# Performance work log

Hardware: AMD Instinct MI355X
Metric: run time of the kernel (lower is better)

## Reference

```python
import jax, jax.numpy as jnp
import numpy as np

M = 16384      # total flat points per role (8 scenes x 2048 pts)
D = 256        # d_model
H = 4          # heads
K = 16         # knn neighbors
DFF = 1024     # 4*D
LN_EPS = 1e-5


def _ln(x, g, b):
    m = jnp.mean(x, axis=-1, keepdims=True)
    v = jnp.mean((x - m) ** 2, axis=-1, keepdims=True)
    return (x - m) / jnp.sqrt(v + LN_EPS) * g + b


def _knn_block(x, coord, ctx, ctx_coord, idx,
               Wq, Wk, Wv, Wo, g1, b1, pe_w, pe_b,
               W1, bf1, W2, bf2, g2, b2):
    # x: [M,D] query feats; ctx: [N,D] context feats; idx: [M,K] neighbor ids (-1 = invalid)
    m, d = x.shape
    k = idx.shape[1]
    dh = d // H
    valid = idx >= 0
    idx_c = jnp.where(valid, idx, 0)

    xn = _ln(x, g1, b1)
    q = (xn @ Wq).reshape(m, H, dh)                      # [M,H,dh]
    k_all = ctx @ Wk                                     # [N,D]
    v_all = ctx @ Wv                                     # [N,D]

    rel = coord[:, None, :] - ctx_coord[idx_c]           # [M,K,3]
    pe = rel @ pe_w + pe_b                               # [M,K,D] relative position encoding
    kg = (k_all[idx_c] + pe).reshape(m, k, H, dh)        # gathered keys  [M,K,H,dh]
    vg = (v_all[idx_c] + pe).reshape(m, k, H, dh)        # gathered values

    scale = jnp.asarray(1.0 / np.sqrt(dh), x.dtype)
    scores = jnp.einsum('mhd,mkhd->mhk', q, kg) * scale
    scores = jnp.where(valid[:, None, :], scores, jnp.asarray(-1e9, x.dtype))
    attn = jax.nn.softmax(scores, axis=-1)
    out = jnp.einsum('mhk,mkhd->mhd', attn, vg).reshape(m, d) @ Wo
    x = x + out
    h = jax.nn.gelu(_ln(x, g2, b2) @ W1 + bf1)
    return x + (h @ W2 + bf2)


def setup_inputs() -> dict:
    key = jax.random.key(0)
    ks = jax.random.split(key, 24)
    s = 0.02
    nblk = 2  # [0]=self(a), [1]=cross(a,b)
    inp = {
        'feat_a': jax.random.normal(ks[0], (M, D), jnp.float32),
        'coord_a': jax.random.normal(ks[1], (M, 3), jnp.float32),
        'feat_b': jax.random.normal(ks[2], (M, D), jnp.float32),
        'coord_b': jax.random.normal(ks[3], (M, 3), jnp.float32),
        'Wq': jax.random.normal(ks[4], (nblk, D, D), jnp.float32) * s,
        'Wk': jax.random.normal(ks[5], (nblk, D, D), jnp.float32) * s,
        'Wv': jax.random.normal(ks[6], (nblk, D, D), jnp.float32) * s,
        'Wo': jax.random.normal(ks[7], (nblk, D, D), jnp.float32) * s,
        'ln1_g': jnp.ones((nblk, D), jnp.float32),
        'ln1_b': jnp.zeros((nblk, D), jnp.float32),
        'pe_w': jax.random.normal(ks[8], (nblk, 3, D), jnp.float32) * s,
        'pe_b': jnp.zeros((nblk, D), jnp.float32),
        'ffn_w1': jax.random.normal(ks[9], (nblk, D, DFF), jnp.float32) * s,
        'ffn_b1': jnp.zeros((nblk, DFF), jnp.float32),
        'ffn_w2': jax.random.normal(ks[10], (nblk, DFF, D), jnp.float32) * s,
        'ffn_b2': jnp.zeros((nblk, D), jnp.float32),
        'ln2_g': jnp.ones((nblk, D), jnp.float32),
        'ln2_b': jnp.zeros((nblk, D), jnp.float32),
        'knn_a2a': jax.random.randint(ks[11], (M, K), 0, M, jnp.int64 if jax.config.jax_enable_x64 else jnp.int32),
        'knn_a2b': jax.random.randint(ks[12], (M, K), 0, M, jnp.int64 if jax.config.jax_enable_x64 else jnp.int32),
    }
    return inp


def reference(feat_a, coord_a, feat_b, coord_b,
              Wq, Wk, Wv, Wo, ln1_g, ln1_b, pe_w, pe_b,
              ffn_w1, ffn_b1, ffn_w2, ffn_b2, ln2_g, ln2_b,
              knn_a2a, knn_a2b):
    def params(i):
        return (Wq[i], Wk[i], Wv[i], Wo[i], ln1_g[i], ln1_b[i], pe_w[i], pe_b[i],
                ffn_w1[i], ffn_b1[i], ffn_w2[i], ffn_b2[i], ln2_g[i], ln2_b[i])
    # layer 'self(a)': feat[a] = block(feat[a], coord[a], knn_indexes['a2a'])
    fa = _knn_block(feat_a, coord_a, feat_a, coord_a, knn_a2a, *params(0))
    # layer 'cross(a,b)': feat[a] = block(query=feat[a], context=feat[b], knn_indexes['a2b'])
    fa = _knn_block(fa, coord_a, feat_b, coord_b, knn_a2b, *params(1))
    return fa
```

## Files before the change

### kernel.cpp

```cpp
#include <hip/hip_runtime.h>
#include <hip/hip_bf16.h>
#include <stdint.h>

#define MM 16384
#define DD 256
#define HH 4
#define KK 16
#define DFF_ 1024

typedef __attribute__((ext_vector_type(8))) short bf16x8;
typedef __attribute__((ext_vector_type(16))) float f32x16;
typedef __attribute__((ext_vector_type(2))) float f32x2;

__device__ __forceinline__ unsigned short f2bf(float f) {
    unsigned u = __builtin_bit_cast(unsigned, f);
    unsigned r = u + 0x7fffu + ((u >> 16) & 1u);
    return (unsigned short)(r >> 16);
}
__device__ __forceinline__ float bf2f(unsigned short h) {
    unsigned u = ((unsigned)h) << 16;
    return __builtin_bit_cast(float, u);
}


__global__ __launch_bounds__(256) void prep_weights(
        const float* __restrict__ Wq, const float* __restrict__ Wk,
        const float* __restrict__ Wv, const float* __restrict__ Wo,
        const float* __restrict__ W1, const float* __restrict__ W2,
        unsigned short* __restrict__ wf) {
    int t = blockIdx.x * blockDim.x + threadIdx.x;
    const float* src; unsigned short* dst;
    int kd, lg, rem, blk, e, sect;
    if (t < 131072) { sect = 0; rem = t; blk = rem >> 16; e = rem & 65535;
        src = Wq; dst = wf + blk * 65536; kd = 256; lg = 8; }
    else if (t < 262144) { sect = 1; rem = t - 131072; blk = rem >> 16; e = rem & 65535;
        src = Wk; dst = wf + 131072 + blk * 131072; kd = 256; lg = 8; }
    else if (t < 393216) { sect = 2; rem = t - 262144; blk = rem >> 16; e = rem & 65535;
        src = Wv; dst = wf + 131072 + blk * 131072; kd = 256; lg = 8; }
    else if (t < 524288) { sect = 0; rem = t - 393216; blk = rem >> 16; e = rem & 65535;
        src = Wo; dst = wf + 393216 + blk * 65536; kd = 256; lg = 8; }
    else if (t < 1048576) { sect = 0; rem = t - 524288; blk = rem >> 18; e = rem & 262143;
        src = W1; dst = wf + 524288 + blk * 262144; kd = 256; lg = 10; }
    else if (t < 1572864) { sect = 0; rem = t - 1048576; blk = rem >> 18; e = rem & 262143;
        src = W2; dst = wf + 1048576 + blk * 262144; kd = 1024; lg = 8; }
    else return;
    int k = e >> lg;
    int n = e & ((1 << lg) - 1);
    if (sect == 1) n = (n >> 2) * 8 + (n & 3);
    else if (sect == 2) n = (n >> 2) * 8 + 4 + (n & 3);
    float v = src[(size_t)blk * kd * (1 << lg) + e];
    int off = ((n >> 5) * (kd >> 4) + (k >> 4)) * 512 + (((k >> 3) & 1) * 32 + (n & 31)) * 8 + (k & 7);
    dst[off] = f2bf(v);
}

__global__ __launch_bounds__(256) void ln3_to_frag(
        const float* __restrict__ xa, const float* __restrict__ g,
        const float* __restrict__ b, const float* __restrict__ xb,
        unsigned short* __restrict__ outln, unsigned short* __restrict__ outca,
        unsigned short* __restrict__ outcb) {
    int y = blockIdx.y;
    const float* x = (y == 2) ? xb : xa;
    unsigned short* out = (y == 0) ? outln : (y == 1 ? outca : outcb);
    int apply_ln = (y == 0);
    int wave = threadIdx.x >> 6, lane = threadIdx.x & 63;
    int m = blockIdx.x * 4 + wave;
    const float4 xv = reinterpret_cast<const float4*>(x + (size_t)m * DD)[lane];
    float vals[4] = {xv.x, xv.y, xv.z, xv.w};
    int k0 = lane * 4;
    if (apply_ln) {
        float s = vals[0] + vals[1] + vals[2] + vals[3];
        float sq = vals[0]*vals[0] + vals[1]*vals[1] + vals[2]*vals[2] + vals[3]*vals[3];
        for (int o = 32; o; o >>= 1) { s += __shfl_xor(s, o, 64); sq += __shfl_xor(sq, o, 64); }
        float mean = s * (1.0f / DD);
        float var = sq * (1.0f / DD) - mean * mean;
        float rs = rsqrtf(var + 1e-5f);
        #pragma unroll
        for (int c = 0; c < 4; ++c)
            vals[c] = (vals[c] - mean) * rs * g[k0 + c] + b[k0 + c];
    }
    int chunk = ((m >> 5) * (DD >> 4) + (k0 >> 4)) * 64 + ((k0 >> 3) & 1) * 32 + (m & 31);
    ushort4 o4 = make_ushort4(f2bf(vals[0]), f2bf(vals[1]), f2bf(vals[2]), f2bf(vals[3]));
    *reinterpret_cast<ushort4*>(out + (size_t)chunk * 8 + (k0 & 7)) = o4;
}

template <int KG>
__device__ __forceinline__ void compute_tile(
        const bf16x8* __restrict__ a0, const bf16x8* __restrict__ a1,
        const bf16x8* __restrict__ b0, const bf16x8* __restrict__ b1,
        f32x16 acc[2][2]) {
    #pragma unroll 4
    for (int g = 0; g < KG; ++g) {
        bf16x8 av0 = a0[g * 64];
        bf16x8 av1 = a1[g * 64];
        bf16x8 bv0 = b0[g * 64];
        bf16x8 bv1 = b1[g * 64];
        acc[0][0] = __builtin_amdgcn_mfma_f32_32x32x16_bf16(av0, bv0, acc[0][0], 0, 0, 0);
        acc[0][1] = __builtin_amdgcn_mfma_f32_32x32x16_bf16(av0, bv1, acc[0][1], 0, 0, 0);
        acc[1][0] = __builtin_amdgcn_mfma_f32_32x32x16_bf16(av1, bv0, acc[1][0], 0, 0, 0);
        acc[1][1] = __builtin_amdgcn_mfma_f32_32x32x16_bf16(av1, bv1, acc[1][1], 0, 0, 0);
    }
}

template <int KD, int NOUT>
__global__ __launch_bounds__(256) void gemm_gelu(
        const bf16x8* __restrict__ A, const bf16x8* __restrict__ B,
        unsigned short* __restrict__ outp, const float* __restrict__ bias,
        int out_kd) {
    constexpr int KG = KD / 16;
    __shared__ float lds[4 * 1056];
    int wave = threadIdx.x >> 6, lane = threadIdx.x & 63;
    int wm = wave & 1, wn = wave >> 1;
    int mw = blockIdx.x * 64 + wm * 32;
    int nw = blockIdx.y * 128 + wn * 64;
    const bf16x8* a0 = A + ((size_t)(mw >> 5) * KG) * 64 + lane;
    const bf16x8* b0 = B + ((size_t)(nw >> 5) * KG) * 64 + lane;
    const bf16x8* b1 = b0 + (size_t)KG * 64;
    f32x16 acc[2] = {};
    #pragma unroll 4
    for (int g = 0; g < KG; ++g) {
        bf16x8 av = a0[g * 64];
        bf16x8 bv0 = b0[g * 64];
        bf16x8 bv1 = b1[g * 64];
        acc[0] = __builtin_amdgcn_mfma_f32_32x32x16_bf16(av, bv0, acc[0], 0, 0, 0);
        acc[1] = __builtin_amdgcn_mfma_f32_32x32x16_bf16(av, bv1, acc[1], 0, 0, 0);
    }
    int col = lane & 31, rq = (lane >> 5) * 4;
    float* wlds = &lds[wave * 1056];
    for (int j = 0; j < 2; ++j) {
        #pragma unroll
        for (int r = 0; r < 16; ++r) {
            int row = (r & 3) + 8 * (r >> 2) + rq;
            int n = nw + j * 32 + col;
            float v = acc[j][r] + bias[n];
            float arg = v * (1.5957691216f + 0.0713548163f * v * v);
            v = v * __frcp_rn(1.0f + __expf(-arg));
            wlds[row * 33 + col] = v;
        }
        #pragma unroll
        for (int it = 0; it < 2; ++it) {
            int task = lane + it * 64;
            int row = task >> 2, cc = task & 3;
            int m = mw + row;
            int k = nw + j * 32 + cc * 8;
            float* p = &wlds[row * 33 + cc * 8];
            unsigned short us[8];
            #pragma unroll
            for (int e = 0; e < 8; ++e) us[e] = f2bf(p[e]);
            int chunk = ((m >> 5) * (out_kd >> 4) + (k >> 4)) * 64 + ((k >> 3) & 1) * 32 + (m & 31);
            reinterpret_cast<uint4*>(outp)[chunk] = *reinterpret_cast<uint4*>(us);
        }
    }
}

template <int KD, int NOUT, bool RESID, bool BIAS>
__global__ __launch_bounds__(256) void gemm_frag64(
        const bf16x8* __restrict__ A, const bf16x8* __restrict__ B,
        float* __restrict__ outp, const float* __restrict__ resid,
        const float* __restrict__ bias) {
    constexpr int KG = KD / 16;
    int wave = threadIdx.x >> 6, lane = threadIdx.x & 63;
    int wm = wave & 1, wn = wave >> 1;
    int mw = blockIdx.x * 64 + wm * 32;
    int nw = blockIdx.y * 128 + wn * 64;
    const bf16x8* a0 = A + ((size_t)(mw >> 5) * KG) * 64 + lane;
    const bf16x8* b0 = B + ((size_t)(nw >> 5) * KG) * 64 + lane;
    const bf16x8* b1 = b0 + (size_t)KG * 64;
    f32x16 acc[2] = {};
    #pragma unroll 4
    for (int g = 0; g < KG; ++g) {
        bf16x8 av = a0[g * 64];
        bf16x8 bv0 = b0[g * 64];
        bf16x8 bv1 = b1[g * 64];
        acc[0] = __builtin_amdgcn_mfma_f32_32x32x16_bf16(av, bv0, acc[0], 0, 0, 0);
        acc[1] = __builtin_amdgcn_mfma_f32_32x32x16_bf16(av, bv1, acc[1], 0, 0, 0);
    }
    int col = lane & 31, rq = (lane >> 5) * 4;
    #pragma unroll
    for (int j = 0; j < 2; ++j) {
        #pragma unroll
        for (int r = 0; r < 16; ++r) {
            int row = (r & 3) + 8 * (r >> 2) + rq;
            int m = mw + row;
            int n = nw + j * 32 + col;
            float v = acc[j][r];
            if (BIAS) v += bias[n];
            if (RESID) v += resid[(size_t)m * NOUT + n];
            outp[(size_t)m * NOUT + n] = v;
        }
    }
}

__global__ __launch_bounds__(256) void gemm_qkv(
        const bf16x8* __restrict__ Aq, const bf16x8* __restrict__ Akv,
        const bf16x8* __restrict__ Bq, const bf16x8* __restrict__ Bkv,
        unsigned short* __restrict__ qout, unsigned char* __restrict__ kvout) {
    constexpr int KG = 16;
    int wave = threadIdx.x >> 6, lane = threadIdx.x & 63;
    int wm = wave & 1, wn = wave >> 1;
    int y = blockIdx.y;
    bool isQ = y < 2;
    const bf16x8* A = isQ ? Aq : Akv;
    const bf16x8* B = isQ ? Bq : Bkv;
    int n0 = (isQ ? y : y - 2) * 128 + wn * 64;
    int m0 = blockIdx.x * 128 + wm * 64;
    const bf16x8* a0 = A + ((size_t)(m0 >> 5) * KG) * 64 + lane;
    const bf16x8* a1 = a0 + (size_t)KG * 64;
    const bf16x8* b0 = B + ((size_t)(n0 >> 5) * KG) * 64 + lane;
    const bf16x8* b1 = b0 + (size_t)KG * 64;
    f32x16 acc[2][2] = {};
    compute_tile<KG>(a0, a1, b0, b1, acc);
    int col = lane & 31, rq = (lane >> 5) * 4;
    #pragma unroll
    for (int i = 0; i < 2; ++i)
    #pragma unroll
    for (int j = 0; j < 2; ++j)
    #pragma unroll
    for (int r = 0; r < 16; ++r) {
        int row = (r & 3) + 8 * (r >> 2) + rq;
        int m = m0 + i * 32 + row;
        int n = n0 + j * 32 + col;
        float v = acc[i][j][r];
        if (isQ) qout[(size_t)m * 256 + n] = f2bf(v);
        else kvout[(size_t)m * 512 + n] =
            (unsigned char)(__builtin_amdgcn_cvt_pk_fp8_f32(v, v, 0, false) & 0xff);
    }
}

template <int O, int N>
__device__ __forceinline__ void redstage(float* a, int lane) {
    int sel = lane & O;
    #pragma unroll
    for (int u = 0; u < N / 2; ++u) {
        float lo = a[2 * u], hi = a[2 * u + 1];
        float keep = sel ? hi : lo;
        float send = sel ? lo : hi;
        a[u] = keep + __shfl_xor(send, O, 64);
    }
}

template <int KD, bool BIAS>
__global__ __launch_bounds__(512) void gemm_ln(
        const bf16x8* __restrict__ A, const bf16x8* __restrict__ B,
        float* __restrict__ out_f32, const float* __restrict__ resid,
        const float* __restrict__ bias,
        const float* __restrict__ lng, const float* __restrict__ lnb,
        unsigned short* __restrict__ out_frag) {
    constexpr int KG = KD / 16;
    __shared__ float pstat[4][64][2];
    __shared__ float stats[64][2];
    __shared__ float tlds[8][32 * 33];
    int wave = threadIdx.x >> 6, lane = threadIdx.x & 63;
    int wm = wave >> 2, wn = wave & 3;
    int m0 = blockIdx.x * 64;
    int mw = m0 + wm * 32;
    int n0 = wn * 64;
    const bf16x8* a0 = A + ((size_t)(mw >> 5) * KG) * 64 + lane;
    const bf16x8* b0 = B + ((size_t)(n0 >> 5) * KG) * 64 + lane;
    const bf16x8* b1 = b0 + (size_t)KG * 64;
    f32x16 acc[2] = {};
    #pragma unroll 4
    for (int g = 0; g < KG; ++g) {
        bf16x8 av = a0[g * 64];
        bf16x8 bv0 = b0[g * 64];
        bf16x8 bv1 = b1[g * 64];
        acc[0] = __builtin_amdgcn_mfma_f32_32x32x16_bf16(av, bv0, acc[0], 0, 0, 0);
        acc[1] = __builtin_amdgcn_mfma_f32_32x32x16_bf16(av, bv1, acc[1], 0, 0, 0);
    }
    int col = lane & 31, rq = (lane >> 5) * 4;

    #pragma unroll
    for (int j = 0; j < 2; ++j) {
        #pragma unroll
        for (int r = 0; r < 16; ++r) {
            int row = (r & 3) + 8 * (r >> 2) + rq;
            int m = mw + row;
            int n = n0 + j * 32 + col;
            float v = acc[j][r];
            if (BIAS) v += bias[n];
            v += resid[(size_t)m * DD + n];
            out_f32[(size_t)m * DD + n] = v;
            acc[j][r] = v;
        }
    }

    {
        float ps[16];
        #pragma unroll
        for (int r = 0; r < 16; ++r)
            ps[r] = acc[0][r] + acc[1][r];
        redstage<1, 16>(ps, lane);
        redstage<2, 8>(ps, lane);
        redstage<4, 4>(ps, lane);
        redstage<8, 2>(ps, lane);
        float sum64 = ps[0] + __shfl_xor(ps[0], 16, 64);
        float qs[16];
        #pragma unroll
        for (int r = 0; r < 16; ++r) {
            float a = acc[0][r], b = acc[1][r];
            qs[r] = a * a + b * b;
        }
        redstage<1, 16>(qs, lane);
        redstage<2, 8>(qs, lane);
        redstage<4, 4>(qs, lane);
        redstage<8, 2>(qs, lane);
        float sq64 = qs[0] + __shfl_xor(qs[0], 16, 64);
        int slot = lane & 15;
        int ROW = wm * 32 + (slot & 3) + 8 * (slot >> 2) + rq;
        if ((lane & 16) == 0)
            *reinterpret_cast<float2*>(&pstat[wn][ROW][0]) = make_float2(sum64, sq64);
    }
    __syncthreads();
    if (threadIdx.x < 64) {
        int R = threadIdx.x;
        float s = 0.0f, sq = 0.0f;
        #pragma unroll
        for (int w = 0; w < 4; ++w) {
            float2 p = *reinterpret_cast<float2*>(&pstat[w][R][0]);
            s += p.x; sq += p.y;
        }
        float mean = s * (1.0f / DD);
        float var = sq * (1.0f / DD) - mean * mean;
        float rstd = rsqrtf(var + 1e-5f);
        *reinterpret_cast<float2*>(&stats[R][0]) = make_float2(mean, rstd);
    }
    __syncthreads();

    float* wlds = &tlds[wave][0];
    float mean_r[16], rstd_r[16];
    #pragma unroll
    for (int r = 0; r < 16; ++r) {
        int row = (r & 3) + 8 * (r >> 2) + rq;
        float2 st = *reinterpret_cast<float2*>(&stats[wm * 32 + row][0]);
        mean_r[r] = st.x; rstd_r[r] = st.y;
    }
    for (int j = 0; j < 2; ++j) {
        float gj = lng[n0 + j * 32 + col];
        float bj = lnb[n0 + j * 32 + col];
        #pragma unroll
        for (int r = 0; r < 16; ++r) {
            int row = (r & 3) + 8 * (r >> 2) + rq;
            float v = (acc[j][r] - mean_r[r]) * rstd_r[r] * gj + bj;
            wlds[row * 33 + col] = v;
        }
        #pragma unroll
        for (int it = 0; it < 2; ++it) {
            int task = lane + it * 64;
            int row = task >> 2, cc = task & 3;
            int m = mw + row;
            int k = n0 + j * 32 + cc * 8;
            float* p = &wlds[row * 33 + cc * 8];
            unsigned short us[8];
            #pragma unroll
            for (int e = 0; e < 8; ++e) us[e] = f2bf(p[e]);
            int chunk = ((m >> 5) * (DD >> 4) + (k >> 4)) * 64 + ((k >> 3) & 1) * 32 + (m & 31);
            *reinterpret_cast<uint4*>(out_frag + (size_t)chunk * 8) = *reinterpret_cast<uint4*>(us);
        }
    }
}

__global__ __launch_bounds__(256) void attn_kernel(
        const unsigned short* __restrict__ q, const unsigned char* __restrict__ kv,
        const float* __restrict__ coord, const float* __restrict__ ctx_coord,
        const int* __restrict__ knn,
        const float* __restrict__ pe_w, const float* __restrict__ pe_b,
        unsigned short* __restrict__ out_frag) {
    int wave = threadIdx.x >> 6, lane = threadIdx.x & 63;
    int m = blockIdx.x * 4 + wave;
    int s = lane & 15;
    int d0 = (lane >> 4) * 64 + s * 4;

    ushort4 qv4 = *reinterpret_cast<const ushort4*>(q + (size_t)m * DD + d0);
    float qx = bf2f(qv4.x), qy = bf2f(qv4.y), qz = bf2f(qv4.z), qw = bf2f(qv4.w);
    float4 pw0 = *reinterpret_cast<const float4*>(pe_w + d0);
    float4 pw1 = *reinterpret_cast<const float4*>(pe_w + DD + d0);
    float4 pw2 = *reinterpret_cast<const float4*>(pe_w + 2 * DD + d0);
    float4 pbv = *reinterpret_cast<const float4*>(pe_b + d0);

    float cx = coord[m * 3], cy = coord[m * 3 + 1], cz = coord[m * 3 + 2];
    int myidx = knn[(size_t)m * KK + s];
    int icm = myidx < 0 ? 0 : myidx;
    float rx = cx - ctx_coord[icm * 3];
    float ry = cy - ctx_coord[icm * 3 + 1];
    float rz = cz - ctx_coord[icm * 3 + 2];

    float t0 = qx * pw0.x + qy * pw0.y + qz * pw0.z + qw * pw0.w;
    float t1 = qx * pw1.x + qy * pw1.y + qz * pw1.z + qw * pw1.w;
    float t2 = qx * pw2.x + qy * pw2.y + qz * pw2.z + qw * pw2.w;
    float t3 = qx * pbv.x + qy * pbv.y + qz * pbv.z + qw * pbv.w;
    #pragma unroll
    for (int o = 1; o < 16; o <<= 1) {
        t0 += __shfl_xor(t0, o, 64);
        t1 += __shfl_xor(t1, o, 64);
        t2 += __shfl_xor(t2, o, 64);
        t3 += __shfl_xor(t3, o, 64);
    }

    float P[KK];
    unsigned vpk[KK];
    #pragma unroll
    for (int j = 0; j < KK; ++j) {
        int ij = __shfl(myidx, j, 64);
        int ic = ij < 0 ? 0 : ij;
        uint2 kvv = *reinterpret_cast<const uint2*>(kv + (size_t)ic * 512 + (d0 >> 2) * 8);
        vpk[j] = kvv.y;
        f32x2 k01 = __builtin_amdgcn_cvt_pk_f32_fp8(kvv.x, false);
        f32x2 k23 = __builtin_amdgcn_cvt_pk_f32_fp8(kvv.x, true);
        P[j] = qx * k01.x + qy * k01.y + qz * k23.x + qw * k23.y;
    }
    redstage<1, 16>(P, lane);
    redstage<2, 8>(P, lane);
    redstage<4, 4>(P, lane);
    redstage<8, 2>(P, lane);
    float corr = rx * t0 + ry * t1 + rz * t2 + t3;
    float sc_own = (myidx >= 0) ? (P[0] + corr) * 0.125f : -1e9f;

    float mx = sc_own;
    mx = fmaxf(mx, __shfl_xor(mx, 1, 64));
    mx = fmaxf(mx, __shfl_xor(mx, 2, 64));
    mx = fmaxf(mx, __shfl_xor(mx, 4, 64));
    mx = fmaxf(mx, __shfl_xor(mx, 8, 64));
    float e = __expf(sc_own - mx);
    float sum = e;
    sum += __shfl_xor(sum, 1, 64);
    sum += __shfl_xor(sum, 2, 64);
    sum += __shfl_xor(sum, 4, 64);
    sum += __shfl_xor(sum, 8, 64);
    float w_own = e * __frcp_rn(sum);

    float wrx = w_own * rx, wry = w_own * ry, wrz = w_own * rz;
    #pragma unroll
    for (int o = 1; o < 16; o <<= 1) {
        wrx += __shfl_xor(wrx, o, 64);
        wry += __shfl_xor(wry, o, 64);
        wrz += __shfl_xor(wrz, o, 64);
    }

    int gbase = lane & 48;
    float ax = 0.f, ay = 0.f, az = 0.f, aw = 0.f;
    #pragma unroll
    for (int j = 0; j < KK; ++j) {
        float wj = __shfl(w_own, gbase + j, 64);
        f32x2 v01 = __builtin_amdgcn_cvt_pk_f32_fp8(vpk[j], false);
        f32x2 v23 = __builtin_amdgcn_cvt_pk_f32_fp8(vpk[j], true);
        ax += wj * v01.x;
        ay += wj * v01.y;
        az += wj * v23.x;
        aw += wj * v23.y;
    }
    ax += wrx * pw0.x + wry * pw1.x + wrz * pw2.x + pbv.x;
    ay += wrx * pw0.y + wry * pw1.y + wrz * pw2.y + pbv.y;
    az += wrx * pw0.z + wry * pw1.z + wrz * pw2.z + pbv.z;
    aw += wrx * pw0.w + wry * pw1.w + wrz * pw2.w + pbv.w;

    ushort4 o4 = make_ushort4(f2bf(ax), f2bf(ay), f2bf(az), f2bf(aw));
    int chunk = ((m >> 5) * (DD >> 4) + (d0 >> 4)) * 64 + ((d0 >> 3) & 1) * 32 + (m & 31);
    *reinterpret_cast<ushort4*>(out_frag + (size_t)chunk * 8 + (d0 & 7)) = o4;
}

extern "C" void kernel_launch(void* const* d_in, const int* in_sizes, int n_in,
                              void* d_out, int out_size, void* d_ws, size_t ws_size,
                              hipStream_t stream) {
    const float* feat_a = (const float*)d_in[0];
    const float* coord_a = (const float*)d_in[1];
    const float* feat_b = (const float*)d_in[2];
    const float* coord_b = (const float*)d_in[3];
    const float* Wq = (const float*)d_in[4];
    const float* Wk = (const float*)d_in[5];
    const float* Wv = (const float*)d_in[6];
    const float* Wo = (const float*)d_in[7];
    const float* ln1_g = (const float*)d_in[8];
    const float* ln1_b = (const float*)d_in[9];
    const float* pe_w = (const float*)d_in[10];
    const float* pe_b = (const float*)d_in[11];
    const float* W1 = (const float*)d_in[12];
    const float* b1 = (const float*)d_in[13];
    const float* W2 = (const float*)d_in[14];
    const float* b2 = (const float*)d_in[15];
    const float* ln2_g = (const float*)d_in[16];
    const float* ln2_b = (const float*)d_in[17];
    const int* knn_a2a = (const int*)d_in[18];
    const int* knn_a2b = (const int*)d_in[19];

    char* ws = (char*)d_ws;
    unsigned short* wfrag = (unsigned short*)ws;
    float* xmid = (float*)(ws + (4ull << 20));
    float* xout0 = (float*)(ws + (20ull << 20));
    unsigned short* qbuf = (unsigned short*)(ws + (36ull << 20));
    unsigned char* kvbuf = (unsigned char*)(ws + (52ull << 20));
    unsigned short* xnf = (unsigned short*)(ws + (68ull << 20));
    unsigned short* ctxfa = (unsigned short*)(ws + (76ull << 20));
    unsigned short* attnf = (unsigned short*)(ws + (84ull << 20));
    unsigned short* ctxfb = (unsigned short*)(ws + (92ull << 20));
    unsigned short* geluf = (unsigned short*)(ws + (36ull << 20));

    const unsigned short* WQF = wfrag;
    const unsigned short* KVF = wfrag + 131072;
    const unsigned short* WOF = wfrag + 393216;
    const unsigned short* W1F = wfrag + 524288;
    const unsigned short* W2F = wfrag + 1048576;

    prep_weights<<<(1572864 + 255) / 256, 256, 0, stream>>>(Wq, Wk, Wv, Wo, W1, W2, wfrag);

    ln3_to_frag<<<dim3(MM / 4, 3), 256, 0, stream>>>(feat_a, ln1_g, ln1_b, feat_b,
                                                     xnf, ctxfa, ctxfb);

    gemm_qkv<<<dim3(MM / 128, 6), 256, 0, stream>>>(
        (const bf16x8*)xnf, (const bf16x8*)ctxfa,
        (const bf16x8*)WQF, (const bf16x8*)KVF, qbuf, kvbuf);

    attn_kernel<<<MM / 4, 256, 0, stream>>>(qbuf, kvbuf, coord_a, coord_a, knn_a2a,
                                            pe_w, pe_b, attnf);

    gemm_ln<256, false><<<MM / 64, 512, 0, stream>>>(
        (const bf16x8*)attnf, (const bf16x8*)WOF, xmid, feat_a, nullptr,
        ln2_g, ln2_b, xnf);

    gemm_gelu<256, 1024><<<dim3(MM / 64, 8), 256, 0, stream>>>(
        (const bf16x8*)xnf, (const bf16x8*)W1F, geluf, b1, 1024);

    gemm_ln<1024, true><<<MM / 64, 512, 0, stream>>>(
        (const bf16x8*)geluf, (const bf16x8*)W2F, xout0, xmid, b2,
        ln1_g + DD, ln1_b + DD, xnf);

    gemm_qkv<<<dim3(MM / 128, 6), 256, 0, stream>>>(
        (const bf16x8*)xnf, (const bf16x8*)ctxfb,
        (const bf16x8*)(WQF + 65536), (const bf16x8*)(KVF + 131072), qbuf, kvbuf);

    attn_kernel<<<MM / 4, 256, 0, stream>>>(qbuf, kvbuf, coord_a, coord_b, knn_a2b,
                                            pe_w + 3 * DD, pe_b + DD, attnf);

    gemm_ln<256, false><<<MM / 64, 512, 0, stream>>>(
        (const bf16x8*)attnf, (const bf16x8*)(WOF + 65536), xmid, xout0, nullptr,
        ln2_g + DD, ln2_b + DD, xnf);

    gemm_gelu<256, 1024><<<dim3(MM / 64, 8), 256, 0, stream>>>(
        (const bf16x8*)xnf, (const bf16x8*)(W1F + 262144), geluf, b1 + DFF_, 1024);

    gemm_frag64<1024, 256, true, true><<<dim3(MM / 64, 2), 256, 0, stream>>>(
        (const bf16x8*)geluf, (const bf16x8*)(W2F + 262144), (float*)d_out, xmid,
        b2 + DD);
}
```

Before: 309.8 us.

## Stage FFN1 GEMM operands through double-buffered LDS with direct global-to-LDS loads

New measurement: 309.4 us. No clear change (-0.1%).

```diff
diff --git a/kernel.cpp b/kernel.cpp
--- a/kernel.cpp
+++ b/kernel.cpp
@@ -20,6 +20,12 @@
 __device__ __forceinline__ float bf2f(unsigned short h) {
     unsigned u = ((unsigned)h) << 16;
     return __builtin_bit_cast(float, u);
+}
+
+__device__ __forceinline__ void gload_lds16(const void* g, void* l) {
+    __builtin_amdgcn_global_load_lds(
+        (const __attribute__((address_space(1))) unsigned int*)g,
+        (__attribute__((address_space(3))) unsigned int*)l, 16, 0, 0);
 }
 
 
@@ -102,36 +108,72 @@
 }
 
 template <int KD, int NOUT>
-__global__ __launch_bounds__(256) void gemm_gelu(
-        const bf16x8* __restrict__ A, const bf16x8* __restrict__ B,
+__global__ __launch_bounds__(256) void gemm_gelu_pipe(
+        const char* __restrict__ A, const char* __restrict__ B,
         unsigned short* __restrict__ outp, const float* __restrict__ bias,
         int out_kd) {
     constexpr int KG = KD / 16;
-    __shared__ float lds[4 * 1056];
+    constexpr int CKG = 4;
+    constexpr int NCH = KG / CKG;
+    __shared__ alignas(16) char smem[2][32768];
     int wave = threadIdx.x >> 6, lane = threadIdx.x & 63;
     int wm = wave & 1, wn = wave >> 1;
-    int mw = blockIdx.x * 64 + wm * 32;
-    int nw = blockIdx.y * 128 + wn * 64;
-    const bf16x8* a0 = A + ((size_t)(mw >> 5) * KG) * 64 + lane;
-    const bf16x8* b0 = B + ((size_t)(nw >> 5) * KG) * 64 + lane;
-    const bf16x8* b1 = b0 + (size_t)KG * 64;
-    f32x16 acc[2] = {};
-    #pragma unroll 4
-    for (int g = 0; g < KG; ++g) {
-        bf16x8 av = a0[g * 64];
-        bf16x8 bv0 = b0[g * 64];
-        bf16x8 bv1 = b1[g * 64];
-        acc[0] = __builtin_amdgcn_mfma_f32_32x32x16_bf16(av, bv0, acc[0], 0, 0, 0);
-        acc[1] = __builtin_amdgcn_mfma_f32_32x32x16_bf16(av, bv1, acc[1], 0, 0, 0);
-    }
+    int m0 = blockIdx.x * 128, n0 = blockIdx.y * 128;
+
+    auto stage = [&](int buf, int c) {
+        #pragma unroll
+        for (int i = 0; i < 8; ++i) {
+            int s = i * 4 + wave;
+            const char* gsrc;
+            if (s < 16) {
+                int g = s >> 2, kk = s & 3;
+                gsrc = A + ((((size_t)(m0 >> 5) + g) * KG + (size_t)c * CKG + kk) << 10);
+            } else {
+                int s2 = s - 16;
+                int g = s2 >> 2, kk = s2 & 3;
+                gsrc = B + ((((size_t)(n0 >> 5) + g) * KG + (size_t)c * CKG + kk) << 10);
+            }
+            gload_lds16(gsrc + lane * 16, &smem[buf][s << 10]);
+        }
+    };
+
+    f32x16 acc[2][2] = {};
+    stage(0, 0);
+    stage(1, 1);
+    #pragma unroll
+    for (int c = 0; c < NCH; ++c) {
+        if (c < NCH - 1) asm volatile("s_waitcnt vmcnt(8)" ::: "memory");
+        else             asm volatile("s_waitcnt vmcnt(0)" ::: "memory");
+        __builtin_amdgcn_s_barrier();
+        const bf16x8* la0 = (const bf16x8*)&smem[c & 1][0] + (2 * wm * CKG) * 64 + lane;
+        const bf16x8* la1 = la0 + CKG * 64;
+        const bf16x8* lb0 = (const bf16x8*)&smem[c & 1][16384] + (2 * wn * CKG) * 64 + lane;
+        const bf16x8* lb1 = lb0 + CKG * 64;
+        #pragma unroll
+        for (int g = 0; g < CKG; ++g) {
+            bf16x8 av0 = la0[g * 64];
+            bf16x8 av1 = la1[g * 64];
+            bf16x8 bv0 = lb0[g * 64];
+            bf16x8 bv1 = lb1[g * 64];
+            acc[0][0] = __builtin_amdgcn_mfma_f32_32x32x16_bf16(av0, bv0, acc[0][0], 0, 0, 0);
+            acc[0][1] = __builtin_amdgcn_mfma_f32_32x32x16_bf16(av0, bv1, acc[0][1], 0, 0, 0);
+            acc[1][0] = __builtin_amdgcn_mfma_f32_32x32x16_bf16(av1, bv0, acc[1][0], 0, 0, 0);
+            acc[1][1] = __builtin_amdgcn_mfma_f32_32x32x16_bf16(av1, bv1, acc[1][1], 0, 0, 0);
+        }
+        __builtin_amdgcn_s_barrier();
+        if (c + 2 < NCH) stage(c & 1, c + 2);
+    }
+
+    int mw = m0 + wm * 64, nw = n0 + wn * 64;
     int col = lane & 31, rq = (lane >> 5) * 4;
-    float* wlds = &lds[wave * 1056];
+    float* wlds = (float*)&smem[0][0] + wave * 1056;
+    for (int i = 0; i < 2; ++i)
     for (int j = 0; j < 2; ++j) {
         #pragma unroll
         for (int r = 0; r < 16; ++r) {
             int row = (r & 3) + 8 * (r >> 2) + rq;
             int n = nw + j * 32 + col;
-            float v = acc[j][r] + bias[n];
+            float v = acc[i][j][r] + bias[n];
             float arg = v * (1.5957691216f + 0.0713548163f * v * v);
             v = v * __frcp_rn(1.0f + __expf(-arg));
             wlds[row * 33 + col] = v;
@@ -140,7 +182,7 @@
         for (int it = 0; it < 2; ++it) {
             int task = lane + it * 64;
             int row = task >> 2, cc = task & 3;
-            int m = mw + row;
+            int m = mw + i * 32 + row;
             int k = nw + j * 32 + cc * 8;
             float* p = &wlds[row * 33 + cc * 8];
             unsigned short us[8];
@@ -515,8 +557,8 @@
         (const bf16x8*)attnf, (const bf16x8*)WOF, xmid, feat_a, nullptr,
         ln2_g, ln2_b, xnf);
 
-    gemm_gelu<256, 1024><<<dim3(MM / 64, 8), 256, 0, stream>>>(
-        (const bf16x8*)xnf, (const bf16x8*)W1F, geluf, b1, 1024);
+    gemm_gelu_pipe<256, 1024><<<dim3(MM / 128, 8), 256, 0, stream>>>(
+        (const char*)xnf, (const char*)W1F, geluf, b1, 1024);
 
     gemm_ln<1024, true><<<MM / 64, 512, 0, stream>>>(
         (const bf16x8*)geluf, (const bf16x8*)W2F, xout0, xmid, b2,
@@ -533,8 +575,8 @@
         (const bf16x8*)attnf, (const bf16x8*)(WOF + 65536), xmid, xout0, nullptr,
         ln2_g + DD, ln2_b + DD, xnf);
 
-    gemm_gelu<256, 1024><<<dim3(MM / 64, 8), 256, 0, stream>>>(
-        (const bf16x8*)xnf, (const bf16x8*)(W1F + 262144), geluf, b1 + DFF_, 1024);
+    gemm_gelu_pipe<256, 1024><<<dim3(MM / 128, 8), 256, 0, stream>>>(
+        (const char*)xnf, (const char*)(W1F + 262144), geluf, b1 + DFF_, 1024);
 
     gemm_frag64<1024, 256, true, true><<<dim3(MM / 64, 2), 256, 0, stream>>>(
         (const bf16x8*)geluf, (const bf16x8*)(W2F + 262144), (float*)d_out, xmid,
```

## Stage FFN1 GEMM operands in LDS via async global-to-LDS loads with larger tiles

Applied to the files above, without the earlier changes.

Result: slower. 318.2 us (+2.7%).

```diff
diff --git a/kernel.cpp b/kernel.cpp
--- a/kernel.cpp
+++ b/kernel.cpp
@@ -20,6 +20,16 @@
 __device__ __forceinline__ float bf2f(unsigned short h) {
     unsigned u = ((unsigned)h) << 16;
     return __builtin_bit_cast(float, u);
+}
+
+__device__ __forceinline__ void gload_lds16(const void* g, void* l) {
+    __builtin_amdgcn_global_load_lds(
+        (const __attribute__((address_space(1))) unsigned int*)g,
+        (__attribute__((address_space(3))) unsigned int*)l, 16, 0, 0);
+}
+
+template <int N> __device__ __forceinline__ void waitv() {
+    asm volatile("s_waitcnt vmcnt(%0)" :: "n"(N) : "memory");
 }
 
 
@@ -101,31 +111,62 @@
     }
 }
 
-template <int KD, int NOUT>
-__global__ __launch_bounds__(256) void gemm_gelu(
-        const bf16x8* __restrict__ A, const bf16x8* __restrict__ B,
+__global__ __launch_bounds__(512) void gemm_gelu_deep(
+        const char* __restrict__ A, const char* __restrict__ B,
         unsigned short* __restrict__ outp, const float* __restrict__ bias,
         int out_kd) {
-    constexpr int KG = KD / 16;
-    __shared__ float lds[4 * 1056];
+    constexpr int KG = 16;
+    __shared__ alignas(16) char smem[131072];
     int wave = threadIdx.x >> 6, lane = threadIdx.x & 63;
-    int wm = wave & 1, wn = wave >> 1;
-    int mw = blockIdx.x * 64 + wm * 32;
-    int nw = blockIdx.y * 128 + wn * 64;
-    const bf16x8* a0 = A + ((size_t)(mw >> 5) * KG) * 64 + lane;
-    const bf16x8* b0 = B + ((size_t)(nw >> 5) * KG) * 64 + lane;
-    const bf16x8* b1 = b0 + (size_t)KG * 64;
+    int wm = wave >> 1, wn = wave & 1;
+    int m0 = blockIdx.x * 128, n0 = blockIdx.y * 128;
+
+    #pragma unroll
+    for (int c = 0; c < 4; ++c) {
+        #pragma unroll
+        for (int i = 0; i < 4; ++i) {
+            int t = wave * 4 + i;
+            const char* gsrc; int s;
+            if (t < 16) {
+                int g = t >> 2; int kg = 4 * c + (t & 3);
+                s = g * 16 + kg;
+                gsrc = A + ((((size_t)(m0 >> 5) + g) * 16 + kg) << 10);
+            } else {
+                int u = t - 16; int g = u >> 2; int kg = 4 * c + (u & 3);
+                s = 64 + g * 16 + kg;
+                gsrc = B + ((((size_t)(n0 >> 5) + g) * 16 + kg) << 10);
+            }
+            gload_lds16(gsrc + lane * 16, smem + ((size_t)s << 10));
+        }
+    }
+
+    const bf16x8* lA  = (const bf16x8*)smem + (wm * 16) * 64 + lane;
+    const bf16x8* lB0 = (const bf16x8*)(smem + 65536) + (wn * 2 * 16) * 64 + lane;
+    const bf16x8* lB1 = lB0 + 16 * 64;
     f32x16 acc[2] = {};
-    #pragma unroll 4
-    for (int g = 0; g < KG; ++g) {
-        bf16x8 av = a0[g * 64];
-        bf16x8 bv0 = b0[g * 64];
-        bf16x8 bv1 = b1[g * 64];
-        acc[0] = __builtin_amdgcn_mfma_f32_32x32x16_bf16(av, bv0, acc[0], 0, 0, 0);
-        acc[1] = __builtin_amdgcn_mfma_f32_32x32x16_bf16(av, bv1, acc[1], 0, 0, 0);
-    }
+
+    #define CHUNK(c, V)                                                         \
+        waitv<V>();                                                             \
+        __builtin_amdgcn_s_barrier();                                           \
+        _Pragma("unroll")                                                       \
+        for (int kg = 4 * (c); kg < 4 * (c) + 4; ++kg) {                        \
+            bf16x8 av  = lA[kg * 64];                                           \
+            bf16x8 bv0 = lB0[kg * 64];                                          \
+            bf16x8 bv1 = lB1[kg * 64];                                          \
+            acc[0] = __builtin_amdgcn_mfma_f32_32x32x16_bf16(av, bv0, acc[0], 0, 0, 0); \
+            acc[1] = __builtin_amdgcn_mfma_f32_32x32x16_bf16(av, bv1, acc[1], 0, 0, 0); \
+        }
+    CHUNK(0, 12)
+    CHUNK(1, 8)
+    CHUNK(2, 4)
+    CHUNK(3, 0)
+    #undef CHUNK
+
+    __builtin_amdgcn_s_barrier();
+
+    int mw = m0 + wm * 32, nw = n0 + wn * 64;
     int col = lane & 31, rq = (lane >> 5) * 4;
-    float* wlds = &lds[wave * 1056];
+    float* wlds = (float*)smem + wave * 1056;
     for (int j = 0; j < 2; ++j) {
         #pragma unroll
         for (int r = 0; r < 16; ++r) {
@@ -515,8 +556,8 @@
         (const bf16x8*)attnf, (const bf16x8*)WOF, xmid, feat_a, nullptr,
         ln2_g, ln2_b, xnf);
 
-    gemm_gelu<256, 1024><<<dim3(MM / 64, 8), 256, 0, stream>>>(
-        (const bf16x8*)xnf, (const bf16x8*)W1F, geluf, b1, 1024);
+    gemm_gelu_deep<<<dim3(MM / 128, 8), 512, 0, stream>>>(
+        (const char*)xnf, (const char*)W1F, geluf, b1, 1024);
 
     gemm_ln<1024, true><<<MM / 64, 512, 0, stream>>>(
         (const bf16x8*)geluf, (const bf16x8*)W2F, xout0, xmid, b2,
@@ -533,8 +574,8 @@
         (const bf16x8*)attnf, (const bf16x8*)(WOF + 65536), xmid, xout0, nullptr,
         ln2_g + DD, ln2_b + DD, xnf);
 
-    gemm_gelu<256, 1024><<<dim3(MM / 64, 8), 256, 0, stream>>>(
-        (const bf16x8*)xnf, (const bf16x8*)(W1F + 262144), geluf, b1 + DFF_, 1024);
+    gemm_gelu_deep<<<dim3(MM / 128, 8), 512, 0, stream>>>(
+        (const char*)xnf, (const char*)(W1F + 262144), geluf, b1 + DFF_, 1024);
 
     gemm_frag64<1024, 256, true, true><<<dim3(MM / 64, 2), 256, 0, stream>>>(
         (const bf16x8*)geluf, (const bf16x8*)(W2F + 262144), (float*)d_out, xmid,
```

## Fuse Wo projection, residual LayerNorm and FFN1 GELU GEMM into one kernel

Applied to the files above, without the earlier changes.

New measurement: 313.1 us. Within noise of the previous version (+1.1%).

```diff
diff --git a/kernel.cpp b/kernel.cpp
--- a/kernel.cpp
+++ b/kernel.cpp
@@ -101,53 +101,180 @@
     }
 }
 
-template <int KD, int NOUT>
-__global__ __launch_bounds__(256) void gemm_gelu(
-        const bf16x8* __restrict__ A, const bf16x8* __restrict__ B,
-        unsigned short* __restrict__ outp, const float* __restrict__ bias,
-        int out_kd) {
-    constexpr int KG = KD / 16;
-    __shared__ float lds[4 * 1056];
+template <int O, int N>
+__device__ __forceinline__ void redstage(float* a, int lane) {
+    int sel = lane & O;
+    #pragma unroll
+    for (int u = 0; u < N / 2; ++u) {
+        float lo = a[2 * u], hi = a[2 * u + 1];
+        float keep = sel ? hi : lo;
+        float send = sel ? lo : hi;
+        a[u] = keep + __shfl_xor(send, O, 64);
+    }
+}
+
+__global__ __launch_bounds__(512) void wo_ln_ffn1(
+        const bf16x8* __restrict__ A, const bf16x8* __restrict__ Bo,
+        float* __restrict__ xmid, const float* __restrict__ resid,
+        const float* __restrict__ lng, const float* __restrict__ lnb,
+        const bf16x8* __restrict__ B1, const float* __restrict__ b1,
+        unsigned short* __restrict__ geluf) {
+    constexpr int KG = 16;
+    __shared__ float pstat[4][64][2];
+    __shared__ float stats[64][2];
+    __shared__ float tlds[8][32 * 33];
+    __shared__ alignas(16) unsigned short xnlds[2][16][64][8];
     int wave = threadIdx.x >> 6, lane = threadIdx.x & 63;
-    int wm = wave & 1, wn = wave >> 1;
-    int mw = blockIdx.x * 64 + wm * 32;
-    int nw = blockIdx.y * 128 + wn * 64;
+    int wm = wave >> 2, wn = wave & 3;
+    int m0 = blockIdx.x * 64;
+    int mw = m0 + wm * 32;
+    int n0 = wn * 64;
     const bf16x8* a0 = A + ((size_t)(mw >> 5) * KG) * 64 + lane;
-    const bf16x8* b0 = B + ((size_t)(nw >> 5) * KG) * 64 + lane;
-    const bf16x8* b1 = b0 + (size_t)KG * 64;
+    const bf16x8* b0 = Bo + ((size_t)(n0 >> 5) * KG) * 64 + lane;
+    const bf16x8* b1o = b0 + (size_t)KG * 64;
     f32x16 acc[2] = {};
     #pragma unroll 4
     for (int g = 0; g < KG; ++g) {
         bf16x8 av = a0[g * 64];
         bf16x8 bv0 = b0[g * 64];
-        bf16x8 bv1 = b1[g * 64];
+        bf16x8 bv1 = b1o[g * 64];
         acc[0] = __builtin_amdgcn_mfma_f32_32x32x16_bf16(av, bv0, acc[0], 0, 0, 0);
         acc[1] = __builtin_amdgcn_mfma_f32_32x32x16_bf16(av, bv1, acc[1], 0, 0, 0);
     }
     int col = lane & 31, rq = (lane >> 5) * 4;
-    float* wlds = &lds[wave * 1056];
+
+    #pragma unroll
     for (int j = 0; j < 2; ++j) {
         #pragma unroll
         for (int r = 0; r < 16; ++r) {
             int row = (r & 3) + 8 * (r >> 2) + rq;
-            int n = nw + j * 32 + col;
-            float v = acc[j][r] + bias[n];
-            float arg = v * (1.5957691216f + 0.0713548163f * v * v);
-            v = v * __frcp_rn(1.0f + __expf(-arg));
-            wlds[row * 33 + col] = v;
-        }
-        #pragma unroll
-        for (int it = 0; it < 2; ++it) {
-            int task = lane + it * 64;
-            int row = task >> 2, cc = task & 3;
             int m = mw + row;
-            int k = nw + j * 32 + cc * 8;
-            float* p = &wlds[row * 33 + cc * 8];
-            unsigned short us[8];
+            int n = n0 + j * 32 + col;
+            float v = acc[j][r];
+            v += resid[(size_t)m * DD + n];
+            xmid[(size_t)m * DD + n] = v;
+            acc[j][r] = v;
+        }
+    }
+
+    {
+        float ps[16];
+        #pragma unroll
+        for (int r = 0; r < 16; ++r) ps[r] = acc[0][r] + acc[1][r];
+        redstage<1, 16>(ps, lane);
+        redstage<2, 8>(ps, lane);
+        redstage<4, 4>(ps, lane);
+        redstage<8, 2>(ps, lane);
+        float sum64 = ps[0] + __shfl_xor(ps[0], 16, 64);
+        float qs[16];
+        #pragma unroll
+        for (int r = 0; r < 16; ++r) {
+            float a = acc[0][r], b = acc[1][r];
+            qs[r] = a * a + b * b;
+        }
+        redstage<1, 16>(qs, lane);
+        redstage<2, 8>(qs, lane);
+        redstage<4, 4>(qs, lane);
+        redstage<8, 2>(qs, lane);
+        float sq64 = qs[0] + __shfl_xor(qs[0], 16, 64);
+        int slot = lane & 15;
+        int ROW = wm * 32 + (slot & 3) + 8 * (slot >> 2) + rq;
+        if ((lane & 16) == 0)
+            *reinterpret_cast<float2*>(&pstat[wn][ROW][0]) = make_float2(sum64, sq64);
+    }
+    __syncthreads();
+    if (threadIdx.x < 64) {
+        int R = threadIdx.x;
+        float s = 0.0f, sq = 0.0f;
+        #pragma unroll
+        for (int w = 0; w < 4; ++w) {
+            float2 p = *reinterpret_cast<float2*>(&pstat[w][R][0]);
+            s += p.x; sq += p.y;
+        }
+        float mean = s * (1.0f / DD);
+        float var = sq * (1.0f / DD) - mean * mean;
+        float rstd = rsqrtf(var + 1e-5f);
+        *reinterpret_cast<float2*>(&stats[R][0]) = make_float2(mean, rstd);
+    }
+    __syncthreads();
+
+    {
+        float* wlds = &tlds[wave][0];
+        float mean_r[16], rstd_r[16];
+        #pragma unroll
+        for (int r = 0; r < 16; ++r) {
+            int row = (r & 3) + 8 * (r >> 2) + rq;
+            float2 st = *reinterpret_cast<float2*>(&stats[wm * 32 + row][0]);
+            mean_r[r] = st.x; rstd_r[r] = st.y;
+        }
+        for (int j = 0; j < 2; ++j) {
+            float gj = lng[n0 + j * 32 + col];
+            float bj = lnb[n0 + j * 32 + col];
             #pragma unroll
-            for (int e = 0; e < 8; ++e) us[e] = f2bf(p[e]);
-            int chunk = ((m >> 5) * (out_kd >> 4) + (k >> 4)) * 64 + ((k >> 3) & 1) * 32 + (m & 31);
-            reinterpret_cast<uint4*>(outp)[chunk] = *reinterpret_cast<uint4*>(us);
+            for (int r = 0; r < 16; ++r) {
+                int row = (r & 3) + 8 * (r >> 2) + rq;
+                float v = (acc[j][r] - mean_r[r]) * rstd_r[r] * gj + bj;
+                wlds[row * 33 + col] = v;
+            }
+            #pragma unroll
+            for (int it = 0; it < 2; ++it) {
+                int task = lane + it * 64;
+                int row = task >> 2, cc = task & 3;
+                int m = mw + row;
+                int k = n0 + j * 32 + cc * 8;
+                float* p = &wlds[row * 33 + cc * 8];
+                unsigned short us[8];
+                #pragma unroll
+                for (int e = 0; e < 8; ++e) us[e] = f2bf(p[e]);
+                int lch = (k >> 4) * 64 + ((k >> 3) & 1) * 32 + (m & 31);
+                reinterpret_cast<uint4*>(&xnlds[wm][0][0][0])[lch] = *reinterpret_cast<uint4*>(us);
+            }
+        }
+    }
+    __syncthreads();
+
+    const bf16x8* la = (const bf16x8*)&xnlds[wm][0][0][0] + lane;
+    #pragma unroll
+    for (int h = 0; h < 2; ++h) {
+        int nw3 = h * 512 + wn * 128;
+        const bf16x8* bb = B1 + ((size_t)(nw3 >> 5) * KG) * 64 + lane;
+        f32x16 acc4[4] = {};
+        #pragma unroll 4
+        for (int g = 0; g < KG; ++g) {
+            bf16x8 av = la[g * 64];
+            bf16x8 bv0 = bb[g * 64];
+            bf16x8 bv1 = bb[(KG + g) * 64];
+            bf16x8 bv2 = bb[(2 * KG + g) * 64];
+            bf16x8 bv3 = bb[(3 * KG + g) * 64];
+            acc4[0] = __builtin_amdgcn_mfma_f32_32x32x16_bf16(av, bv0, acc4[0], 0, 0, 0);
+            acc4[1] = __builtin_amdgcn_mfma_f32_32x32x16_bf16(av, bv1, acc4[1], 0, 0, 0);
+            acc4[2] = __builtin_amdgcn_mfma_f32_32x32x16_bf16(av, bv2, acc4[2], 0, 0, 0);
+            acc4[3] = __builtin_amdgcn_mfma_f32_32x32x16_bf16(av, bv3, acc4[3], 0, 0, 0);
+        }
+        float* wlds = &tlds[wave][0];
+        for (int j = 0; j < 4; ++j) {
+            #pragma unroll
+            for (int r = 0; r < 16; ++r) {
+                int row = (r & 3) + 8 * (r >> 2) + rq;
+                int n = nw3 + j * 32 + col;
+                float v = acc4[j][r] + b1[n];
+                float arg = v * (1.5957691216f + 0.0713548163f * v * v);
+                v = v * __frcp_rn(1.0f + __expf(-arg));
+                wlds[row * 33 + col] = v;
+            }
+            #pragma unroll
+            for (int it = 0; it < 2; ++it) {
+                int task = lane + it * 64;
+                int row = task >> 2, cc = task & 3;
+                int m = mw + row;
+                int k = nw3 + j * 32 + cc * 8;
+                float* p = &wlds[row * 33 + cc * 8];
+                unsigned short us[8];
+                #pragma unroll
+                for (int e = 0; e < 8; ++e) us[e] = f2bf(p[e]);
+                int chunk = ((m >> 5) * (DFF_ >> 4) + (k >> 4)) * 64 + ((k >> 3) & 1) * 32 + (m & 31);
+                reinterpret_cast<uint4*>(geluf)[chunk] = *reinterpret_cast<uint4*>(us);
+            }
         }
     }
 }
@@ -223,18 +350,6 @@
         if (isQ) qout[(size_t)m * 256 + n] = f2bf(v);
         else kvout[(size_t)m * 512 + n] =
             (unsigned char)(__builtin_amdgcn_cvt_pk_fp8_f32(v, v, 0, false) & 0xff);
-    }
-}
-
-template <int O, int N>
-__device__ __forceinline__ void redstage(float* a, int lane) {
-    int sel = lane & O;
-    #pragma unroll
-    for (int u = 0; u < N / 2; ++u) {
-        float lo = a[2 * u], hi = a[2 * u + 1];
-        float keep = sel ? hi : lo;
-        float send = sel ? lo : hi;
-        a[u] = keep + __shfl_xor(send, O, 64);
     }
 }
 
@@ -511,12 +626,9 @@
     attn_kernel<<<MM / 4, 256, 0, stream>>>(qbuf, kvbuf, coord_a, coord_a, knn_a2a,
                                             pe_w, pe_b, attnf);
 
-    gemm_ln<256, false><<<MM / 64, 512, 0, stream>>>(
-        (const bf16x8*)attnf, (const bf16x8*)WOF, xmid, feat_a, nullptr,
-        ln2_g, ln2_b, xnf);
-
-    gemm_gelu<256, 1024><<<dim3(MM / 64, 8), 256, 0, stream>>>(
-        (const bf16x8*)xnf, (const bf16x8*)W1F, geluf, b1, 1024);
+    wo_ln_ffn1<<<MM / 64, 512, 0, stream>>>(
+        (const bf16x8*)attnf, (const bf16x8*)WOF, xmid, feat_a,
+        ln2_g, ln2_b, (const bf16x8*)W1F, b1, geluf);
 
     gemm_ln<1024, true><<<MM / 64, 512, 0, stream>>>(
         (const bf16x8*)geluf, (const bf16x8*)W2F, xout0, xmid, b2,
@@ -529,12 +641,9 @@
     attn_kernel<<<MM / 4, 256, 0, stream>>>(qbuf, kvbuf, coord_a, coord_b, knn_a2b,
                                             pe_w + 3 * DD, pe_b + DD, attnf);
 
-    gemm_ln<256, false><<<MM / 64, 512, 0, stream>>>(
-        (const bf16x8*)attnf, (const bf16x8*)(WOF + 65536), xmid, xout0, nullptr,
-        ln2_g + DD, ln2_b + DD, xnf);
-
-    gemm_gelu<256, 1024><<<dim3(MM / 64, 8), 256, 0, stream>>>(
-        (const bf16x8*)xnf, (const bf16x8*)(W1F + 262144), geluf, b1 + DFF_, 1024);
+    wo_ln_ffn1<<<MM / 64, 512, 0, stream>>>(
+        (const bf16x8*)attnf, (const bf16x8*)(WOF + 65536), xmid, xout0,
+        ln2_g + DD, ln2_b + DD, (const bf16x8*)(W1F + 262144), b1 + DFF_, geluf);
 
     gemm_frag64<1024, 256, true, true><<<dim3(MM / 64, 2), 256, 0, stream>>>(
         (const bf16x8*)geluf, (const bf16x8*)(W2F + 262144), (float*)d_out, xmid,
```
